# Optimization experiments

Measured on AMD Instinct MI355X. Metric: run time of the kernel, lower is better.

Reference implementation:

```python
import jax, jax.numpy as jnp
import numpy as np

B, N, DIM = 8, 2048, 1024
EPSILON = 0.03
SCALE = 1.0 / np.sqrt(DIM).astype(np.float32)


def setup_inputs() -> dict:
    key = jax.random.key(0)
    ks = jax.random.split(key, 5)
    Q = jax.random.normal(ks[0], (B, N, DIM), dtype=jnp.float32)
    K = jax.random.normal(ks[1], (B, N, DIM), dtype=jnp.float32)
    V = jax.random.normal(ks[2], (B, N, DIM), dtype=jnp.float32)
    # H_net: Linear(dim, dim//2) -> SiLU -> Linear(dim//2, 1); init like torch default scale-ish
    W1 = jax.random.normal(ks[3], (DIM, DIM // 2), dtype=jnp.float32) * (1.0 / np.sqrt(DIM))
    b1 = jnp.zeros((DIM // 2,), dtype=jnp.float32)
    W2 = jax.random.normal(ks[4], (DIM // 2, 1), dtype=jnp.float32) * (1.0 / np.sqrt(DIM // 2))
    b2 = jnp.zeros((1,), dtype=jnp.float32)
    return {"Q": Q, "K": K, "V": V, "W1": W1, "b1": b1, "W2": W2, "b2": b2}


def _mlp(x, W1, b1, W2, b2):
    h = jax.nn.silu(x @ W1 + b1)  # [B,N,dim//2]
    return h @ W2 + b2            # [B,N,1]


def reference(Q, K, V, W1, b1, W2, b2):
    def energy(q, v):
        # scores [B,N,N]
        A = jax.nn.softmax(jnp.einsum('bnd,bmd->bnm', q, K) * SCALE, axis=-1)
        attn_out = jnp.einsum('bnm,bmd->bnd', A, v)
        H = jnp.sum(_mlp(attn_out, W1, b1, W2, b2))
        return H, attn_out

    # grads of scalar energy H w.r.t. Q and V (dH_dV is computed per the
    # original code but discarded by the final split; only dH_dQ survives)
    (dH_dQ, dH_dV), attn_out = jax.grad(energy, argnums=(0, 1), has_aux=True)(Q, V)
    # S_new = cat([Q,V]) + eps*cat([dH_dV, -dH_dQ]); split -> V_new = V - eps*dH_dQ
    V_new = V - EPSILON * dH_dQ
    return V_new + attn_out
```

## Files before the change

kernel.cpp:

```cpp
#include <hip/hip_runtime.h>

typedef __bf16 bf16;
typedef __attribute__((ext_vector_type(8))) __bf16 bf16x8;
typedef __attribute__((ext_vector_type(4))) float f32x4;

#define MEMFENCE asm volatile("" ::: "memory")

__device__ __forceinline__ void gload16(const bf16* g, bf16* l) {
    __builtin_amdgcn_global_load_lds(
        (const __attribute__((address_space(1))) void*)g,
        (__attribute__((address_space(3))) void*)l,
        16, 0, 0);
}

template<int EPI>
__global__ __launch_bounds__(512, 1)
void gemm8p(const bf16* __restrict__ A, const bf16* __restrict__ Bm,
            void* __restrict__ Cp, int Kdim, int lda, int ldb, int ldc,
            long sA, long sB, long sC, float alpha,
            const float* __restrict__ aux1, const bf16* __restrict__ aux3)
{
    __shared__ __align__(16) char smem[163840];

    const int gx = gridDim.x, gy = gridDim.y;
    int lin = blockIdx.x + gx * (blockIdx.y + gy * blockIdx.z);
    const int q = (gx * gy * gridDim.z) >> 3;
    lin = (lin & 7) * q + (lin >> 3);
    const int bx = lin % gx;
    const int rem0 = lin / gx;
    const int by = rem0 % gy;
    const int bz = rem0 / gy;

    const int t0 = threadIdx.x;
    const int w = t0 >> 6, lane = t0 & 63;
    const int wm = w >> 2, wn = w & 3;
    const int m0 = by * 256, n0 = bx * 256;
    const long zb = bz;

    const bf16* Ab = A  + zb * sA + (size_t)m0 * lda;
    const bf16* Bb = Bm + zb * sB + (size_t)n0 * ldb;

    const int sr16 = lane >> 2;
    const int sce  = ((((lane & 3) << 4) ^ (((lane >> 5) & 1) << 5))) >> 1;
    const int r0s = (w >> 1) * 16 + sr16;
    const int c0s = (w & 1) * 32 + sce;
    const bf16* gA0 = Ab + (size_t)r0s * lda + c0s;
    const bf16* gA1 = Ab + (size_t)(128 + r0s) * lda + c0s;
    const bf16* gB0 = Bb + (size_t)r0s * ldb + c0s;
    const bf16* gB1 = Bb + (size_t)(128 + r0s) * ldb + c0s;
    const size_t a64 = (size_t)64 * lda, b64 = (size_t)64 * ldb;
    const int ldsW0 = w * 1024, ldsW1 = (8 + w) * 1024;

    const int lr = lane & 15, lkq = lane >> 4;
    const int phx = ((lane >> 3) & 1) << 5;
    const int frag_base = (lr * 64 + lkq * 16) ^ phx;
    const char* aR = smem + wm * 16384 + frag_base;
    const char* bR = smem + 98304 + (wn >> 1) * 16384 + (wn & 1) * 8192 + frag_base;

    f32x4 acc[8][4] = {};
    const int NTt = Kdim >> 6;

    auto stgA = [&](int h, int u, int off) {
        char* L = smem + off + h * 16384;
        const bf16* g = h ? gA1 : gA0;
        gload16(g + (size_t)u * 64,        (bf16*)(L + ldsW0));
        gload16(g + a64 + (size_t)u * 64,  (bf16*)(L + ldsW1));
    };
    auto stgB = [&](int h, int u, int p) {
        char* L = smem + 98304 + p * 32768 + h * 16384;
        const bf16* g = h ? gB1 : gB0;
        gload16(g + (size_t)u * 64,        (bf16*)(L + ldsW0));
        gload16(g + b64 + (size_t)u * 64,  (bf16*)(L + ldsW1));
    };

    stgA(0, 0, 0);     stgA(1, 0, 0);     stgB(0, 0, 0); stgB(1, 0, 0);
    stgA(0, 1, 32768); stgA(1, 1, 32768); stgB(0, 1, 1); stgB(1, 1, 1);
    asm volatile("s_waitcnt vmcnt(8)" ::: "memory");
    __builtin_amdgcn_s_barrier();
    MEMFENCE;

    bf16x8 a[4][2], bl[2][2], bh[2][2];
    #pragma unroll
    for (int mf = 0; mf < 4; ++mf)
        #pragma unroll
        for (int ks = 0; ks < 2; ++ks)
            a[mf][ks] = *(const bf16x8*)(aR + (mf * 2 + ks) * 1024);
    #pragma unroll
    for (int nf = 0; nf < 2; ++nf)
        #pragma unroll
        for (int ks = 0; ks < 2; ++ks)
            bh[nf][ks] = *(const bf16x8*)(bR + ((2 + nf) * 2 + ks) * 1024);

#define QUADQ(MFB, NFB, AARR, BARR)                                                     \
    __builtin_amdgcn_s_setprio(1);                                                      \
    _Pragma("unroll")                                                                   \
    for (int ks = 0; ks < 2; ++ks)                                                      \
        _Pragma("unroll")                                                               \
        for (int mf = 0; mf < 4; ++mf)                                                  \
            _Pragma("unroll")                                                           \
            for (int nf = 0; nf < 2; ++nf)                                              \
                acc[(MFB) + mf][(NFB) + nf] = __builtin_amdgcn_mfma_f32_16x16x32_bf16(  \
                    AARR[mf][ks], BARR[nf][ks], acc[(MFB) + mf][(NFB) + nf], 0, 0, 0);  \
    __builtin_amdgcn_s_setprio(0);

    int aOff = 0, aOff1 = 32768, sOff = 65536;
    for (int u = 0; u < NTt; ++u) {
        const int p = u & 1;
        const char* aP  = aR + aOff;
        const char* aP1 = aR + aOff1;
        const char* bP  = bR + p * 32768;
        const char* bP1 = bR + (p ^ 1) * 32768;
        const bool st2 = (u + 2 < NTt), nx = (u + 1 < NTt);

        if (st2) stgA(0, u + 2, sOff);
        #pragma unroll
        for (int nf = 0; nf < 2; ++nf)
            #pragma unroll
            for (int ks = 0; ks < 2; ++ks)
                bl[nf][ks] = *(const bf16x8*)(bP + (nf * 2 + ks) * 1024);
        QUADQ(0, 2, a, bh)

        if (st2) stgA(1, u + 2, sOff);
        QUADQ(0, 0, a, bl)
        #pragma unroll
        for (int mf = 0; mf < 4; ++mf)
            #pragma unroll
            for (int ks = 0; ks < 2; ++ks)
                a[mf][ks] = *(const bf16x8*)(aP + ((4 + mf) * 2 + ks) * 1024);
        MEMFENCE;
        if (st2)     asm volatile("s_waitcnt vmcnt(4)" ::: "memory");
        else if (nx) asm volatile("s_waitcnt vmcnt(0)" ::: "memory");
        __builtin_amdgcn_s_barrier();
        MEMFENCE;

        if (st2) stgB(0, u + 2, p);
        QUADQ(4, 0, a, bl)

        if (st2) stgB(1, u + 2, p);
        QUADQ(4, 2, a, bh)
        if (nx) {
            #pragma unroll
            for (int mf = 0; mf < 4; ++mf)
                #pragma unroll
                for (int ks = 0; ks < 2; ++ks)
                    a[mf][ks] = *(const bf16x8*)(aP1 + (mf * 2 + ks) * 1024);
            #pragma unroll
            for (int nf = 0; nf < 2; ++nf)
                #pragma unroll
                for (int ks = 0; ks < 2; ++ks)
                    bh[nf][ks] = *(const bf16x8*)(bP1 + ((2 + nf) * 2 + ks) * 1024);
        }
        MEMFENCE;
        __builtin_amdgcn_s_barrier();
        MEMFENCE;

        const int tmp = aOff; aOff = aOff1; aOff1 = sOff; sOff = tmp;
    }
#undef QUADQ

    const int rb  = m0 + wm * 128 + lkq * 4;
    const int cb0 = n0 + wn * 64 + lr;
    #pragma unroll
    for (int mf = 0; mf < 8; ++mf) {
        #pragma unroll
        for (int r = 0; r < 4; ++r) {
            const int rw = rb + mf * 16 + r;
            float rd = 0.f;
            if (EPI == 1) {
                const size_t gr = zb * 2048 + rw;
                rd = aux1[gr] + aux1[16384 + gr] + aux1[32768 + gr] + aux1[49152 + gr];
            }
            #pragma unroll
            for (int nf = 0; nf < 4; ++nf) {
                const int c = cb0 + nf * 16;
                const size_t ix = (size_t)rw * ldc + c;
                const float v = acc[mf][nf][r];
                if (EPI == 0) {
                    ((bf16*)Cp + zb * sC)[ix] = (bf16)(alpha * v);
                } else if (EPI == 1) {
                    bf16* Cb = (bf16*)Cp + zb * sC;
                    const bf16* Am = aux3 + zb * sC;
                    Cb[ix] = (bf16)((float)Am[ix] * (v - rd));
                } else {
                    float* C = (float*)Cp + zb * sC;
                    const float* Vv = aux1 + zb * sC;
                    const bf16* AOv = aux3 + zb * sC;
                    C[ix] = Vv[ix] + (float)AOv[ix] - alpha * v;
                }
            }
        }
    }
}

template<int EPI, int NF>
__global__ __launch_bounds__(512, 1)
void gemm_nc(const bf16* __restrict__ A, const bf16* __restrict__ Bm,
             void* __restrict__ Cp, int Kdim, int lda, int ldb, int ldc,
             long sA, long sB, long sC, float alpha,
             const float* __restrict__ aux1, const float* __restrict__ aux2,
             float* __restrict__ rds)
{
    constexpr int SB = NF * 4096;
    __shared__ __align__(16) char smem[65536 + 4 * SB];

    const int gx = gridDim.x, gy = gridDim.y;
    int lin = blockIdx.x + gx * (blockIdx.y + gy * blockIdx.z);
    const int q = (gx * gy * gridDim.z) >> 3;
    lin = (lin & 7) * q + (lin >> 3);
    const int bx = lin % gx;
    const int rem0 = lin / gx;
    const int by = rem0 % gy;
    const int bz = rem0 / gy;

    const int t0 = threadIdx.x;
    const int w = t0 >> 6, lane = t0 & 63;
    const int wm = w >> 2, wn = w & 3;
    const int m0 = by * 256, n0 = bx * (64 * NF);
    const long zb = bz;

    const bf16* Ab = A  + zb * sA + (size_t)m0 * lda;
    const bf16* Bb = Bm + zb * sB + (size_t)n0 * ldb;

    const int sr16 = lane >> 2;
    const int sce  = ((((lane & 3) << 4) ^ (((lane >> 5) & 1) << 5))) >> 1;
    const int stg0 = w * 2, stg1 = w * 2 + 1;
    const bf16* pA0 = Ab + (size_t)(stg0 * 16 + sr16) * lda + sce;
    const bf16* pA1 = Ab + (size_t)(stg1 * 16 + sr16) * lda + sce;
    const bf16* pB0 = Bb + (size_t)((NF == 4 ? stg0 : w) * 16 + sr16) * ldb + sce;
    const bf16* pB1 = Bb + (size_t)(stg1 * 16 + sr16) * ldb + sce;

    const int lr = lane & 15, lkq = lane >> 4;
    const int phx = ((lane >> 3) & 1) << 5;
    const int frag_base = lr * 64 + lkq * 16;

    f32x4 acc[8][NF] = {};
    const int NT = Kdim >> 5;

    auto issueSlot = [&](int p) {
        char* lA = smem + (p & 3) * 16384;
        char* lB = smem + 65536 + (p & 3) * SB;
        const int kt = p << 5;
        gload16(pA0 + kt, (bf16*)(lA + stg0 * 1024));
        gload16(pA1 + kt, (bf16*)(lA + stg1 * 1024));
        if (NF == 4) {
            gload16(pB0 + kt, (bf16*)(lB + stg0 * 1024));
            gload16(pB1 + kt, (bf16*)(lB + stg1 * 1024));
        } else {
            gload16(pB0 + kt, (bf16*)(lB + w * 1024));
        }
    };
    auto rdA = [&](const char* base, int sub) {
        return *(const bf16x8*)(base + (((sub << 10) + frag_base) ^ phx));
    };

    issueSlot(0); issueSlot(1); issueSlot(2);
    if (NF == 4) asm volatile("s_waitcnt vmcnt(4)" ::: "memory");
    else         asm volatile("s_waitcnt vmcnt(3)" ::: "memory");
    __builtin_amdgcn_s_barrier();
    MEMFENCE;

    bf16x8 alo[4], ahi[4], b0[NF], b1[NF];
    {
        const char* cA = smem;
        const char* cB = smem + 65536;
        #pragma unroll
        for (int mf = 0; mf < 4; ++mf) alo[mf] = rdA(cA, wm * 8 + mf);
        #pragma unroll
        for (int nf = 0; nf < NF; ++nf) b0[nf] = rdA(cB, wn * NF + nf);
    }

    auto stepBody = [&](int SL, int s, bf16x8 (&bA)[NF], bf16x8 (&bB)[NF]) {
        if (s + 3 < NT) issueSlot(s + 3);
        const char* cA = smem + SL * 16384;
        #pragma unroll
        for (int mf = 0; mf < 4; ++mf) ahi[mf] = rdA(cA, wm * 8 + 4 + mf);

        __builtin_amdgcn_s_setprio(1);
        #pragma unroll
        for (int mf = 0; mf < 4; ++mf)
            #pragma unroll
            for (int nf = 0; nf < NF; ++nf)
                acc[mf][nf] = __builtin_amdgcn_mfma_f32_16x16x32_bf16(alo[mf], bA[nf], acc[mf][nf], 0, 0, 0);
        __builtin_amdgcn_s_setprio(0);

        if (s + 1 < NT) {
            const int NS = (SL + 1) & 3;
            const char* nA = smem + NS * 16384;
            const char* nB = smem + 65536 + NS * SB;
            #pragma unroll
            for (int mf = 0; mf < 4; ++mf) alo[mf] = rdA(nA, wm * 8 + mf);
            #pragma unroll
            for (int nf = 0; nf < NF; ++nf) bB[nf] = rdA(nB, wn * NF + nf);
        }

        __builtin_amdgcn_s_setprio(1);
        #pragma unroll
        for (int mf = 0; mf < 4; ++mf)
            #pragma unroll
            for (int nf = 0; nf < NF; ++nf)
                acc[4 + mf][nf] = __builtin_amdgcn_mfma_f32_16x16x32_bf16(ahi[mf], bA[nf], acc[4 + mf][nf], 0, 0, 0);
        __builtin_amdgcn_s_setprio(0);

        MEMFENCE;
        if (s + 3 < NT) {
            if (NF == 4) asm volatile("s_waitcnt vmcnt(4)" ::: "memory");
            else         asm volatile("s_waitcnt vmcnt(3)" ::: "memory");
        } else {
            asm volatile("s_waitcnt vmcnt(0)" ::: "memory");
        }
        __builtin_amdgcn_s_barrier();
        MEMFENCE;
    };

    for (int s = 0; s < NT; s += 2) {
        stepBody(s & 3, s, b0, b1);
        stepBody((s + 1) & 3, s + 1, b1, b0);
    }

    const int rb  = m0 + wm * 128 + lkq * 4;
    const int cb0 = n0 + wn * (NF * 16) + lr;

    if (EPI == 0) {
        #pragma unroll
        for (int mf = 0; mf < 8; ++mf)
            #pragma unroll
            for (int nf = 0; nf < NF; ++nf) {
                const int c = cb0 + nf * 16;
                #pragma unroll
                for (int r = 0; r < 4; ++r) {
                    const int rw = rb + mf * 16 + r;
                    ((bf16*)Cp + zb * sC)[(size_t)rw * ldc + c] = (bf16)(alpha * acc[mf][nf][r]);
                }
            }
    } else {
        float* smemF = (float*)smem;
        #pragma unroll
        for (int mf = 0; mf < 8; ++mf) {
            #pragma unroll
            for (int r = 0; r < 4; ++r) {
                const int rw = rb + mf * 16 + r;
                float pd = 0.f;
                #pragma unroll
                for (int nf = 0; nf < NF; ++nf) {
                    const int c = cb0 + nf * 16;
                    const float v = acc[mf][nf][r];
                    const float u = v + aux1[c];
                    const float sg = 1.f / (1.f + __expf(-u));
                    const float dd = sg * (1.f + u * (1.f - sg));
                    const float uval = dd * aux2[c];
                    ((bf16*)Cp)[(size_t)rw * ldc + c] = (bf16)uval;
                    pd += uval * v;
                }
                #pragma unroll
                for (int o = 1; o < 16; o <<= 1) pd += __shfl_xor(pd, o, 64);
                if (lr == 0)
                    smemF[wn * 256 + wm * 128 + mf * 16 + lkq * 4 + r] = pd;
            }
        }
        __syncthreads();
        if (t0 < 256) {
            const float s4 = smemF[t0] + smemF[256 + t0] + smemF[512 + t0] + smemF[768 + t0];
            rds[(size_t)bx * 16384 + m0 + t0] = s4;
        }
    }
}

template<bool DN, bool DT>
__device__ __forceinline__ void transcast_body(
                 const float* __restrict__ in, bf16* __restrict__ outN,
                 bf16* __restrict__ outT, int R, int C, int bx, int by, int bz,
                 float (*ts)[65])
{
    const int t = threadIdx.x;
    const int c0 = bx * 64, r0 = by * 64;
    const size_t zoff = (size_t)bz * R * C;

    const int rr = t >> 2, cc = (t & 3) * 16;
    float4 f[4];
    const float* src = in + zoff + (size_t)(r0 + rr) * C + c0 + cc;
    #pragma unroll
    for (int i = 0; i < 4; ++i) f[i] = *(const float4*)(src + 4 * i);

    if (DN) {
        bf16x8 h0, h1;
        #pragma unroll
        for (int i = 0; i < 2; ++i) {
            h0[i*4+0] = (bf16)f[i].x;   h0[i*4+1] = (bf16)f[i].y;
            h0[i*4+2] = (bf16)f[i].z;   h0[i*4+3] = (bf16)f[i].w;
            h1[i*4+0] = (bf16)f[i+2].x; h1[i*4+1] = (bf16)f[i+2].y;
            h1[i*4+2] = (bf16)f[i+2].z; h1[i*4+3] = (bf16)f[i+2].w;
        }
        bf16* dst = outN + zoff + (size_t)(r0 + rr) * C + c0 + cc;
        *(bf16x8*)dst = h0;
        *(bf16x8*)(dst + 8) = h1;
    }
    if (DT) {
        #pragma unroll
        for (int i = 0; i < 4; ++i) {
            ts[rr][cc + 4*i + 0] = f[i].x;
            ts[rr][cc + 4*i + 1] = f[i].y;
            ts[rr][cc + 4*i + 2] = f[i].z;
            ts[rr][cc + 4*i + 3] = f[i].w;
        }
        __syncthreads();
        const int ct = t >> 2, rr4 = (t & 3) * 16;
        bf16x8 o0, o1;
        #pragma unroll
        for (int i = 0; i < 8; ++i) o0[i] = (bf16)ts[rr4 + i][ct];
        #pragma unroll
        for (int i = 0; i < 8; ++i) o1[i] = (bf16)ts[rr4 + 8 + i][ct];
        bf16* dst = outT + zoff + (size_t)(c0 + ct) * R + r0 + rr4;
        *(bf16x8*)dst = o0;
        *(bf16x8*)(dst + 8) = o1;
    }
}

__global__ __launch_bounds__(256)
void trans_all(const float* __restrict__ Q, const float* __restrict__ Km,
               const float* __restrict__ V, const float* __restrict__ W1,
               bf16* __restrict__ Qb, bf16* __restrict__ Kb, bf16* __restrict__ KbT,
               bf16* __restrict__ Vb, bf16* __restrict__ VbT, bf16* __restrict__ W1T)
{
    __shared__ float ts[64][65];
    const int z = blockIdx.z;
    if (z < 8) {
        transcast_body<true, false>(Q, Qb, nullptr, 2048, 1024, blockIdx.x, blockIdx.y, z, ts);
    } else if (z < 16) {
        transcast_body<true, true>(Km, Kb, KbT, 2048, 1024, blockIdx.x, blockIdx.y, z - 8, ts);
    } else if (z < 24) {
        transcast_body<true, true>(V, Vb, VbT, 2048, 1024, blockIdx.x, blockIdx.y, z - 16, ts);
    } else {
        if (blockIdx.x < 8 && blockIdx.y < 16)
            transcast_body<false, true>(W1, nullptr, W1T, 1024, 512, blockIdx.x, blockIdx.y, 0, ts);
    }
}

__global__ __launch_bounds__(256)
void softmax_k(const bf16* __restrict__ S, bf16* __restrict__ A)
{
    const size_t row = blockIdx.x;
    const int t = threadIdx.x;
    const int wid = t >> 6, lane = t & 63;
    __shared__ float r1[4], r2[4];

    bf16x8 v = *(const bf16x8*)(S + row * 2048 + t * 8);
    float f[8];
    float mx = -1e30f;
    #pragma unroll
    for (int i = 0; i < 8; ++i) { f[i] = (float)v[i]; mx = fmaxf(mx, f[i]); }
    #pragma unroll
    for (int o = 32; o; o >>= 1) mx = fmaxf(mx, __shfl_xor(mx, o, 64));
    if (!lane) r1[wid] = mx;
    __syncthreads();
    mx = fmaxf(fmaxf(r1[0], r1[1]), fmaxf(r1[2], r1[3]));

    float sum = 0.f;
    #pragma unroll
    for (int i = 0; i < 8; ++i) { f[i] = __expf(f[i] - mx); sum += f[i]; }
    #pragma unroll
    for (int o = 32; o; o >>= 1) sum += __shfl_xor(sum, o, 64);
    if (!lane) r2[wid] = sum;
    __syncthreads();
    sum = r2[0] + r2[1] + r2[2] + r2[3];

    const float inv = 1.f / sum;
    bf16x8 ov;
    #pragma unroll
    for (int i = 0; i < 8; ++i) ov[i] = (bf16)(f[i] * inv);
    *(bf16x8*)(A + row * 2048 + t * 8) = ov;
}

extern "C" void kernel_launch(void* const* d_in, const int* in_sizes, int n_in,
                              void* d_out, int out_size, void* d_ws, size_t ws_size,
                              hipStream_t stream)
{
    const float* Q  = (const float*)d_in[0];
    const float* Km = (const float*)d_in[1];
    const float* V  = (const float*)d_in[2];
    const float* W1 = (const float*)d_in[3];
    const float* b1 = (const float*)d_in[4];
    const float* W2 = (const float*)d_in[5];
    float* out = (float*)d_out;

    char* ws = (char*)d_ws;
    bf16* Amat = (bf16*)(ws);
    bf16* AO   = (bf16*)(ws + 67108864);
    bf16* Kb   = AO;
    bf16* KbT  = (bf16*)(ws + 100663296);
    bf16* Vb   = (bf16*)(ws + 134217728);
    float* rdSlab = (float*)(ws + 134217728);
    bf16* VbT  = (bf16*)(ws + 167772160);
    bf16* U    = VbT;
    bf16* Qb   = (bf16*)(ws + 201326592);
    bf16* VW1b = Qb;
    bf16* W1T  = (bf16*)(ws + 234881024);
    bf16* S    = (bf16*)d_out;

    const long sQK = 2048L * 1024;
    const long sS  = 2048L * 2048;
    const long sVW = 2048L * 512;
    dim3 blk(256), blkG(512);

    trans_all<<<dim3(16, 32, 25), blk, 0, stream>>>(Q, Km, V, W1, Qb, Kb, KbT, Vb, VbT, W1T);

    gemm8p<0><<<dim3(8, 8, 8), blkG, 0, stream>>>(
        Qb, Kb, S, 1024, 1024, 1024, 2048, sQK, sQK, sS, 0.03125f, nullptr, nullptr);

    gemm_nc<0, 2><<<dim3(4, 8, 8), blkG, 0, stream>>>(
        Vb, W1T, VW1b, 1024, 1024, 1024, 512, sQK, 0, sVW, 1.0f, nullptr, nullptr, nullptr);

    softmax_k<<<dim3(16384), blk, 0, stream>>>(S, Amat);

    gemm8p<0><<<dim3(4, 8, 8), blkG, 0, stream>>>(
        Amat, VbT, AO, 2048, 2048, 2048, 1024, sS, sQK, sQK, 1.0f, nullptr, nullptr);

    gemm_nc<3, 2><<<dim3(4, 64, 1), blkG, 0, stream>>>(
        AO, W1T, U, 1024, 1024, 1024, 512, 0, 0, 0, 1.0f, b1, W2, rdSlab);

    gemm8p<1><<<dim3(8, 8, 8), blkG, 0, stream>>>(
        U, VW1b, Amat, 512, 512, 512, 2048, sVW, sVW, sS, 1.0f, rdSlab, Amat);

    gemm8p<2><<<dim3(4, 8, 8), blkG, 0, stream>>>(
        Amat, KbT, out, 2048, 2048, 2048, 1024, sS, sQK, sQK, 0.03f * 0.03125f, V, AO);
}
```

Baseline: 405.6 us.

## Run backward-path GEMMs in FP8 with scaled operands and FP8 intermediates

```diff
diff --git a/kernel.cpp b/kernel.cpp
--- a/kernel.cpp
+++ b/kernel.cpp
@@ -1,25 +1,32 @@
 #include <hip/hip_runtime.h>
 
 typedef __bf16 bf16;
+typedef long i64;
 typedef __attribute__((ext_vector_type(8))) __bf16 bf16x8;
 typedef __attribute__((ext_vector_type(4))) float f32x4;
+typedef __attribute__((ext_vector_type(4))) int i32x4;
 
 #define MEMFENCE asm volatile("" ::: "memory")
 
-__device__ __forceinline__ void gload16(const bf16* g, bf16* l) {
+__device__ __forceinline__ unsigned char tofp8(float x) {
+    return (unsigned char)(__builtin_amdgcn_cvt_pk_fp8_f32(x, x, 0, false) & 0xff);
+}
+
+__device__ __forceinline__ void gload16(const void* g, void* l) {
     __builtin_amdgcn_global_load_lds(
         (const __attribute__((address_space(1))) void*)g,
         (__attribute__((address_space(3))) void*)l,
         16, 0, 0);
 }
 
-template<int EPI>
+template<int EPI, int F8>
 __global__ __launch_bounds__(512, 1)
-void gemm8p(const bf16* __restrict__ A, const bf16* __restrict__ Bm,
+void gemm8p(const void* __restrict__ A, const void* __restrict__ Bm,
             void* __restrict__ Cp, int Kdim, int lda, int ldb, int ldc,
             long sA, long sB, long sC, float alpha,
             const float* __restrict__ aux1, const bf16* __restrict__ aux3)
 {
+    constexpr int ES = F8 ? 1 : 2;
     __shared__ __align__(16) char smem[163840];
 
     const int gx = gridDim.x, gy = gridDim.y;
@@ -37,40 +44,43 @@
     const int m0 = by * 256, n0 = bx * 256;
     const long zb = bz;
 
-    const bf16* Ab = A  + zb * sA + (size_t)m0 * lda;
-    const bf16* Bb = Bm + zb * sB + (size_t)n0 * ldb;
+    const char* Ab = (const char*)A + ((size_t)zb * sA + (size_t)m0 * lda) * ES;
+    const char* Bb = (const char*)Bm + ((size_t)zb * sB + (size_t)n0 * ldb) * ES;
 
     const int sr16 = lane >> 2;
-    const int sce  = ((((lane & 3) << 4) ^ (((lane >> 5) & 1) << 5))) >> 1;
+    const int sceB = F8 ? ((((lane & 3) ^ (sr16 & 3) ^ (((lane >> 5) & 1) << 1)) << 4))
+                        : ((((lane & 3) << 4) ^ (((lane >> 5) & 1) << 5)));
     const int r0s = (w >> 1) * 16 + sr16;
-    const int c0s = (w & 1) * 32 + sce;
-    const bf16* gA0 = Ab + (size_t)r0s * lda + c0s;
-    const bf16* gA1 = Ab + (size_t)(128 + r0s) * lda + c0s;
-    const bf16* gB0 = Bb + (size_t)r0s * ldb + c0s;
-    const bf16* gB1 = Bb + (size_t)(128 + r0s) * ldb + c0s;
-    const size_t a64 = (size_t)64 * lda, b64 = (size_t)64 * ldb;
+    const int c0sB = (w & 1) * 64 + sceB;
+    const char* gA0 = Ab + (size_t)r0s * lda * ES + c0sB;
+    const char* gA1 = Ab + (size_t)(128 + r0s) * lda * ES + c0sB;
+    const char* gB0 = Bb + (size_t)r0s * ldb * ES + c0sB;
+    const char* gB1 = Bb + (size_t)(128 + r0s) * ldb * ES + c0sB;
+    const size_t a64 = (size_t)64 * lda * ES, b64 = (size_t)64 * ldb * ES;
     const int ldsW0 = w * 1024, ldsW1 = (8 + w) * 1024;
 
     const int lr = lane & 15, lkq = lane >> 4;
     const int phx = ((lane >> 3) & 1) << 5;
-    const int frag_base = (lr * 64 + lkq * 16) ^ phx;
+    const int frag_base = F8 ? (lr * 64) : ((lr * 64 + lkq * 16) ^ phx);
+    const int e0 = (((0 + (lkq >> 1)) ^ (lr & 3) ^ (((lr >> 3) & 1) << 1)) << 4) + ((lkq & 1) << 3);
+    const int e1 = (((2 + (lkq >> 1)) ^ (lr & 3) ^ (((lr >> 3) & 1) << 1)) << 4) + ((lkq & 1) << 3);
     const char* aR = smem + wm * 16384 + frag_base;
     const char* bR = smem + 98304 + (wn >> 1) * 16384 + (wn & 1) * 8192 + frag_base;
 
     f32x4 acc[8][4] = {};
-    const int NTt = Kdim >> 6;
+    const int NTt = Kdim >> (F8 ? 7 : 6);
 
     auto stgA = [&](int h, int u, int off) {
         char* L = smem + off + h * 16384;
-        const bf16* g = h ? gA1 : gA0;
-        gload16(g + (size_t)u * 64,        (bf16*)(L + ldsW0));
-        gload16(g + a64 + (size_t)u * 64,  (bf16*)(L + ldsW1));
+        const char* g = h ? gA1 : gA0;
+        gload16(g + (size_t)u * 128,        L + ldsW0);
+        gload16(g + a64 + (size_t)u * 128,  L + ldsW1);
     };
     auto stgB = [&](int h, int u, int p) {
         char* L = smem + 98304 + p * 32768 + h * 16384;
-        const bf16* g = h ? gB1 : gB0;
-        gload16(g + (size_t)u * 64,        (bf16*)(L + ldsW0));
-        gload16(g + b64 + (size_t)u * 64,  (bf16*)(L + ldsW1));
+        const char* g = h ? gB1 : gB0;
+        gload16(g + (size_t)u * 128,        L + ldsW0);
+        gload16(g + b64 + (size_t)u * 128,  L + ldsW1);
     };
 
     stgA(0, 0, 0);     stgA(1, 0, 0);     stgB(0, 0, 0); stgB(1, 0, 0);
@@ -80,16 +90,33 @@
     MEMFENCE;
 
     bf16x8 a[4][2], bl[2][2], bh[2][2];
-    #pragma unroll
-    for (int mf = 0; mf < 4; ++mf)
-        #pragma unroll
-        for (int ks = 0; ks < 2; ++ks)
-            a[mf][ks] = *(const bf16x8*)(aR + (mf * 2 + ks) * 1024);
-    #pragma unroll
-    for (int nf = 0; nf < 2; ++nf)
-        #pragma unroll
-        for (int ks = 0; ks < 2; ++ks)
-            bh[nf][ks] = *(const bf16x8*)(bR + ((2 + nf) * 2 + ks) * 1024);
+    i64 a8[4][2][2], bl8[2][2][2], bh8[2][2][2];
+
+#define RD8(DST, BASE, SUB)                                                \
+    DST[0] = *(const i64*)((BASE) + (SUB) * 1024 + e0);                    \
+    DST[1] = *(const i64*)((BASE) + (SUB) * 1024 + e1);
+
+    if constexpr (!F8) {
+        #pragma unroll
+        for (int mf = 0; mf < 4; ++mf)
+            #pragma unroll
+            for (int ks = 0; ks < 2; ++ks)
+                a[mf][ks] = *(const bf16x8*)(aR + (mf * 2 + ks) * 1024);
+        #pragma unroll
+        for (int nf = 0; nf < 2; ++nf)
+            #pragma unroll
+            for (int ks = 0; ks < 2; ++ks)
+                bh[nf][ks] = *(const bf16x8*)(bR + ((2 + nf) * 2 + ks) * 1024);
+    } else {
+        #pragma unroll
+        for (int mf = 0; mf < 4; ++mf)
+            #pragma unroll
+            for (int ks = 0; ks < 2; ++ks) { RD8(a8[mf][ks], aR, mf * 2 + ks) }
+        #pragma unroll
+        for (int nf = 0; nf < 2; ++nf)
+            #pragma unroll
+            for (int ks = 0; ks < 2; ++ks) { RD8(bh8[nf][ks], bR, (2 + nf) * 2 + ks) }
+    }
 
 #define QUADQ(MFB, NFB, AARR, BARR)                                                     \
     __builtin_amdgcn_s_setprio(1);                                                      \
@@ -103,6 +130,22 @@
                     AARR[mf][ks], BARR[nf][ks], acc[(MFB) + mf][(NFB) + nf], 0, 0, 0);  \
     __builtin_amdgcn_s_setprio(0);
 
+#define QUAD8(MFB, NFB, AARR, BARR)                                                     \
+    __builtin_amdgcn_s_setprio(1);                                                      \
+    _Pragma("unroll")                                                                   \
+    for (int ks = 0; ks < 2; ++ks)                                                      \
+        _Pragma("unroll")                                                               \
+        for (int k2 = 0; k2 < 2; ++k2)                                                  \
+            _Pragma("unroll")                                                           \
+            for (int mf = 0; mf < 4; ++mf)                                              \
+                _Pragma("unroll")                                                       \
+                for (int nf = 0; nf < 2; ++nf)                                          \
+                    acc[(MFB) + mf][(NFB) + nf] =                                       \
+                        __builtin_amdgcn_mfma_f32_16x16x32_fp8_fp8(                     \
+                            AARR[mf][ks][k2], BARR[nf][ks][k2],                         \
+                            acc[(MFB) + mf][(NFB) + nf], 0, 0, 0);                      \
+    __builtin_amdgcn_s_setprio(0);
+
     int aOff = 0, aOff1 = 32768, sOff = 65536;
     for (int u = 0; u < NTt; ++u) {
         const int p = u & 1;
@@ -113,20 +156,36 @@
         const bool st2 = (u + 2 < NTt), nx = (u + 1 < NTt);
 
         if (st2) stgA(0, u + 2, sOff);
-        #pragma unroll
-        for (int nf = 0; nf < 2; ++nf)
-            #pragma unroll
-            for (int ks = 0; ks < 2; ++ks)
-                bl[nf][ks] = *(const bf16x8*)(bP + (nf * 2 + ks) * 1024);
-        QUADQ(0, 2, a, bh)
+        if constexpr (!F8) {
+            #pragma unroll
+            for (int nf = 0; nf < 2; ++nf)
+                #pragma unroll
+                for (int ks = 0; ks < 2; ++ks)
+                    bl[nf][ks] = *(const bf16x8*)(bP + (nf * 2 + ks) * 1024);
+            QUADQ(0, 2, a, bh)
+        } else {
+            #pragma unroll
+            for (int nf = 0; nf < 2; ++nf)
+                #pragma unroll
+                for (int ks = 0; ks < 2; ++ks) { RD8(bl8[nf][ks], bP, nf * 2 + ks) }
+            QUAD8(0, 2, a8, bh8)
+        }
 
         if (st2) stgA(1, u + 2, sOff);
-        QUADQ(0, 0, a, bl)
-        #pragma unroll
-        for (int mf = 0; mf < 4; ++mf)
-            #pragma unroll
-            for (int ks = 0; ks < 2; ++ks)
-                a[mf][ks] = *(const bf16x8*)(aP + ((4 + mf) * 2 + ks) * 1024);
+        if constexpr (!F8) {
+            QUADQ(0, 0, a, bl)
+            #pragma unroll
+            for (int mf = 0; mf < 4; ++mf)
+                #pragma unroll
+                for (int ks = 0; ks < 2; ++ks)
+                    a[mf][ks] = *(const bf16x8*)(aP + ((4 + mf) * 2 + ks) * 1024);
+        } else {
+            QUAD8(0, 0, a8, bl8)
+            #pragma unroll
+            for (int mf = 0; mf < 4; ++mf)
+                #pragma unroll
+                for (int ks = 0; ks < 2; ++ks) { RD8(a8[mf][ks], aP, (4 + mf) * 2 + ks) }
+        }
         MEMFENCE;
         if (st2)     asm volatile("s_waitcnt vmcnt(4)" ::: "memory");
         else if (nx) asm volatile("s_waitcnt vmcnt(0)" ::: "memory");
@@ -134,21 +193,35 @@
         MEMFENCE;
 
         if (st2) stgB(0, u + 2, p);
-        QUADQ(4, 0, a, bl)
+        if constexpr (!F8) { QUADQ(4, 0, a, bl) } else { QUAD8(4, 0, a8, bl8) }
 
         if (st2) stgB(1, u + 2, p);
-        QUADQ(4, 2, a, bh)
-        if (nx) {
-            #pragma unroll
-            for (int mf = 0; mf < 4; ++mf)
-                #pragma unroll
-                for (int ks = 0; ks < 2; ++ks)
-                    a[mf][ks] = *(const bf16x8*)(aP1 + (mf * 2 + ks) * 1024);
-            #pragma unroll
-            for (int nf = 0; nf < 2; ++nf)
-                #pragma unroll
-                for (int ks = 0; ks < 2; ++ks)
-                    bh[nf][ks] = *(const bf16x8*)(bP1 + ((2 + nf) * 2 + ks) * 1024);
+        if constexpr (!F8) {
+            QUADQ(4, 2, a, bh)
+            if (nx) {
+                #pragma unroll
+                for (int mf = 0; mf < 4; ++mf)
+                    #pragma unroll
+                    for (int ks = 0; ks < 2; ++ks)
+                        a[mf][ks] = *(const bf16x8*)(aP1 + (mf * 2 + ks) * 1024);
+                #pragma unroll
+                for (int nf = 0; nf < 2; ++nf)
+                    #pragma unroll
+                    for (int ks = 0; ks < 2; ++ks)
+                        bh[nf][ks] = *(const bf16x8*)(bP1 + ((2 + nf) * 2 + ks) * 1024);
+            }
+        } else {
+            QUAD8(4, 2, a8, bh8)
+            if (nx) {
+                #pragma unroll
+                for (int mf = 0; mf < 4; ++mf)
+                    #pragma unroll
+                    for (int ks = 0; ks < 2; ++ks) { RD8(a8[mf][ks], aP1, mf * 2 + ks) }
+                #pragma unroll
+                for (int nf = 0; nf < 2; ++nf)
+                    #pragma unroll
+                    for (int ks = 0; ks < 2; ++ks) { RD8(bh8[nf][ks], bP1, (2 + nf) * 2 + ks) }
+            }
         }
         MEMFENCE;
         __builtin_amdgcn_s_barrier();
@@ -157,6 +230,8 @@
         const int tmp = aOff; aOff = aOff1; aOff1 = sOff; sOff = tmp;
     }
 #undef QUADQ
+#undef QUAD8
+#undef RD8
 
     const int rb  = m0 + wm * 128 + lkq * 4;
     const int cb0 = n0 + wn * 64 + lr;
@@ -178,9 +253,9 @@
                 if (EPI == 0) {
                     ((bf16*)Cp + zb * sC)[ix] = (bf16)(alpha * v);
                 } else if (EPI == 1) {
-                    bf16* Cb = (bf16*)Cp + zb * sC;
                     const bf16* Am = aux3 + zb * sC;
-                    Cb[ix] = (bf16)((float)Am[ix] * (v - rd));
+                    const float t = (float)Am[ix] * (v * alpha - rd) * 64.f;
+                    ((unsigned char*)Cp + zb * sC)[ix] = tofp8(t);
                 } else {
                     float* C = (float*)Cp + zb * sC;
                     const float* Vv = aux1 + zb * sC;
@@ -240,13 +315,13 @@
         char* lA = smem + (p & 3) * 16384;
         char* lB = smem + 65536 + (p & 3) * SB;
         const int kt = p << 5;
-        gload16(pA0 + kt, (bf16*)(lA + stg0 * 1024));
-        gload16(pA1 + kt, (bf16*)(lA + stg1 * 1024));
+        gload16(pA0 + kt, lA + stg0 * 1024);
+        gload16(pA1 + kt, lA + stg1 * 1024);
         if (NF == 4) {
-            gload16(pB0 + kt, (bf16*)(lB + stg0 * 1024));
-            gload16(pB1 + kt, (bf16*)(lB + stg1 * 1024));
+            gload16(pB0 + kt, lB + stg0 * 1024);
+            gload16(pB1 + kt, lB + stg1 * 1024);
         } else {
-            gload16(pB0 + kt, (bf16*)(lB + w * 1024));
+            gload16(pB0 + kt, lB + w * 1024);
         }
     };
     auto rdA = [&](const char* base, int sub) {
@@ -320,7 +395,7 @@
     const int rb  = m0 + wm * 128 + lkq * 4;
     const int cb0 = n0 + wn * (NF * 16) + lr;
 
-    if (EPI == 0) {
+    if (EPI == 0 || EPI == 4) {
         #pragma unroll
         for (int mf = 0; mf < 8; ++mf)
             #pragma unroll
@@ -329,7 +404,11 @@
                 #pragma unroll
                 for (int r = 0; r < 4; ++r) {
                     const int rw = rb + mf * 16 + r;
-                    ((bf16*)Cp + zb * sC)[(size_t)rw * ldc + c] = (bf16)(alpha * acc[mf][nf][r]);
+                    const size_t ix = (size_t)rw * ldc + c;
+                    if (EPI == 0)
+                        ((bf16*)Cp + zb * sC)[ix] = (bf16)(alpha * acc[mf][nf][r]);
+                    else
+                        ((unsigned char*)Cp + zb * sC)[ix] = tofp8(alpha * acc[mf][nf][r]);
                 }
             }
     } else {
@@ -348,7 +427,7 @@
                     const float sg = 1.f / (1.f + __expf(-u));
                     const float dd = sg * (1.f + u * (1.f - sg));
                     const float uval = dd * aux2[c];
-                    ((bf16*)Cp)[(size_t)rw * ldc + c] = (bf16)uval;
+                    ((unsigned char*)Cp)[(size_t)rw * ldc + c] = tofp8(uval * 16.f);
                     pd += uval * v;
                 }
                 #pragma unroll
@@ -365,10 +444,10 @@
     }
 }
 
-template<bool DN, bool DT>
+template<bool DN, int TM>
 __device__ __forceinline__ void transcast_body(
                  const float* __restrict__ in, bf16* __restrict__ outN,
-                 bf16* __restrict__ outT, int R, int C, int bx, int by, int bz,
+                 void* __restrict__ outT, int R, int C, int bx, int by, int bz,
                  float (*ts)[65])
 {
     const int t = threadIdx.x;
@@ -394,7 +473,7 @@
         *(bf16x8*)dst = h0;
         *(bf16x8*)(dst + 8) = h1;
     }
-    if (DT) {
+    if (TM) {
         #pragma unroll
         for (int i = 0; i < 4; ++i) {
             ts[rr][cc + 4*i + 0] = f[i].x;
@@ -404,34 +483,46 @@
         }
         __syncthreads();
         const int ct = t >> 2, rr4 = (t & 3) * 16;
-        bf16x8 o0, o1;
-        #pragma unroll
-        for (int i = 0; i < 8; ++i) o0[i] = (bf16)ts[rr4 + i][ct];
-        #pragma unroll
-        for (int i = 0; i < 8; ++i) o1[i] = (bf16)ts[rr4 + 8 + i][ct];
-        bf16* dst = outT + zoff + (size_t)(c0 + ct) * R + r0 + rr4;
-        *(bf16x8*)dst = o0;
-        *(bf16x8*)(dst + 8) = o1;
+        if (TM == 1) {
+            bf16x8 o0, o1;
+            #pragma unroll
+            for (int i = 0; i < 8; ++i) o0[i] = (bf16)ts[rr4 + i][ct];
+            #pragma unroll
+            for (int i = 0; i < 8; ++i) o1[i] = (bf16)ts[rr4 + 8 + i][ct];
+            bf16* dst = (bf16*)outT + zoff + (size_t)(c0 + ct) * R + r0 + rr4;
+            *(bf16x8*)dst = o0;
+            *(bf16x8*)(dst + 8) = o1;
+        } else {
+            i32x4 o;
+            #pragma unroll
+            for (int g = 0; g < 4; ++g) {
+                int v = __builtin_amdgcn_cvt_pk_fp8_f32(ts[rr4 + 4*g + 0][ct], ts[rr4 + 4*g + 1][ct], 0, false);
+                v = __builtin_amdgcn_cvt_pk_fp8_f32(ts[rr4 + 4*g + 2][ct], ts[rr4 + 4*g + 3][ct], v, true);
+                o[g] = v;
+            }
+            unsigned char* dst = (unsigned char*)outT + zoff + (size_t)(c0 + ct) * R + r0 + rr4;
+            *(i32x4*)dst = o;
+        }
     }
 }
 
 __global__ __launch_bounds__(256)
 void trans_all(const float* __restrict__ Q, const float* __restrict__ Km,
                const float* __restrict__ V, const float* __restrict__ W1,
-               bf16* __restrict__ Qb, bf16* __restrict__ Kb, bf16* __restrict__ KbT,
+               bf16* __restrict__ Qb, bf16* __restrict__ Kb, unsigned char* __restrict__ KbT8,
                bf16* __restrict__ Vb, bf16* __restrict__ VbT, bf16* __restrict__ W1T)
 {
     __shared__ float ts[64][65];
     const int z = blockIdx.z;
     if (z < 8) {
-        transcast_body<true, false>(Q, Qb, nullptr, 2048, 1024, blockIdx.x, blockIdx.y, z, ts);
+        transcast_body<true, 0>(Q, Qb, nullptr, 2048, 1024, blockIdx.x, blockIdx.y, z, ts);
     } else if (z < 16) {
-        transcast_body<true, true>(Km, Kb, KbT, 2048, 1024, blockIdx.x, blockIdx.y, z - 8, ts);
+        transcast_body<true, 2>(Km, Kb, KbT8, 2048, 1024, blockIdx.x, blockIdx.y, z - 8, ts);
     } else if (z < 24) {
-        transcast_body<true, true>(V, Vb, VbT, 2048, 1024, blockIdx.x, blockIdx.y, z - 16, ts);
+        transcast_body<true, 1>(V, Vb, VbT, 2048, 1024, blockIdx.x, blockIdx.y, z - 16, ts);
     } else {
         if (blockIdx.x < 8 && blockIdx.y < 16)
-            transcast_body<false, true>(W1, nullptr, W1T, 1024, 512, blockIdx.x, blockIdx.y, 0, ts);
+            transcast_body<false, 1>(W1, nullptr, W1T, 1024, 512, blockIdx.x, blockIdx.y, 0, ts);
     }
 }
 
@@ -486,13 +577,14 @@
     bf16* Amat = (bf16*)(ws);
     bf16* AO   = (bf16*)(ws + 67108864);
     bf16* Kb   = AO;
-    bf16* KbT  = (bf16*)(ws + 100663296);
+    unsigned char* KbT8 = (unsigned char*)(ws + 100663296);
+    float* rdSlab = (float*)(ws + 117440512);
     bf16* Vb   = (bf16*)(ws + 134217728);
-    float* rdSlab = (float*)(ws + 134217728);
+    unsigned char* dS8 = (unsigned char*)(ws + 134217728);
     bf16* VbT  = (bf16*)(ws + 167772160);
-    bf16* U    = VbT;
+    unsigned char* U8 = (unsigned char*)(ws + 167772160);
     bf16* Qb   = (bf16*)(ws + 201326592);
-    bf16* VW1b = Qb;
+    unsigned char* VW18 = (unsigned char*)(ws + 201326592);
     bf16* W1T  = (bf16*)(ws + 234881024);
     bf16* S    = (bf16*)d_out;
 
@@ -501,25 +593,26 @@
     const long sVW = 2048L * 512;
     dim3 blk(256), blkG(512);
 
-    trans_all<<<dim3(16, 32, 25), blk, 0, stream>>>(Q, Km, V, W1, Qb, Kb, KbT, Vb, VbT, W1T);
-
-    gemm8p<0><<<dim3(8, 8, 8), blkG, 0, stream>>>(
+    trans_all<<<dim3(16, 32, 25), blk, 0, stream>>>(Q, Km, V, W1, Qb, Kb, KbT8, Vb, VbT, W1T);
+
+    gemm8p<0, 0><<<dim3(8, 8, 8), blkG, 0, stream>>>(
         Qb, Kb, S, 1024, 1024, 1024, 2048, sQK, sQK, sS, 0.03125f, nullptr, nullptr);
 
-    gemm_nc<0, 2><<<dim3(4, 8, 8), blkG, 0, stream>>>(
-        Vb, W1T, VW1b, 1024, 1024, 1024, 512, sQK, 0, sVW, 1.0f, nullptr, nullptr, nullptr);
+    gemm_nc<4, 2><<<dim3(4, 8, 8), blkG, 0, stream>>>(
+        Vb, W1T, VW18, 1024, 1024, 1024, 512, sQK, 0, sVW, 1.0f, nullptr, nullptr, nullptr);
 
     softmax_k<<<dim3(16384), blk, 0, stream>>>(S, Amat);
 
-    gemm8p<0><<<dim3(4, 8, 8), blkG, 0, stream>>>(
+    gemm8p<0, 0><<<dim3(4, 8, 8), blkG, 0, stream>>>(
         Amat, VbT, AO, 2048, 2048, 2048, 1024, sS, sQK, sQK, 1.0f, nullptr, nullptr);
 
     gemm_nc<3, 2><<<dim3(4, 64, 1), blkG, 0, stream>>>(
-        AO, W1T, U, 1024, 1024, 1024, 512, 0, 0, 0, 1.0f, b1, W2, rdSlab);
-
-    gemm8p<1><<<dim3(8, 8, 8), blkG, 0, stream>>>(
-        U, VW1b, Amat, 512, 512, 512, 2048, sVW, sVW, sS, 1.0f, rdSlab, Amat);
-
-    gemm8p<2><<<dim3(4, 8, 8), blkG, 0, stream>>>(
-        Amat, KbT, out, 2048, 2048, 2048, 1024, sS, sQK, sQK, 0.03f * 0.03125f, V, AO);
-}
+        AO, W1T, U8, 1024, 1024, 1024, 512, 0, 0, 0, 1.0f, b1, W2, rdSlab);
+
+    gemm8p<1, 1><<<dim3(8, 8, 8), blkG, 0, stream>>>(
+        U8, VW18, dS8, 512, 512, 512, 2048, 1048576, 1048576, 4194304, 0.0625f, rdSlab, Amat);
+
+    gemm8p<2, 1><<<dim3(4, 8, 8), blkG, 0, stream>>>(
+        dS8, KbT8, out, 2048, 2048, 2048, 1024, 4194304, 2097152, 2097152,
+        0.03f * 0.03125f / 64.f, V, AO);
+}
```

New measurement: 402.5 us. No clear change (-0.8%).
